# Performance work log

Hardware: AMD Instinct MI355X
Metric: run time of the kernel (lower is better)

Reference implementation:

```python
import jax, jax.numpy as jnp
import numpy as np

N_USER = 200000
N_TITEM = 200000  # sized >= N_USER because original code indexes ti_emb with user ids (faithful to source bug)
D = 256           # embed_dim
H = 128           # hidden = embed_dim // 2
N_HID = 2         # config.layers - 1 extra hidden blocks
B = 65536


def setup_inputs() -> dict:
    key = jax.random.key(0)
    ks = jax.random.split(key, 10)
    sc_d = 1.0 / np.sqrt(D)
    sc_h = 1.0 / np.sqrt(H)
    return {
        "user": jax.random.randint(ks[0], (B,), 0, N_USER),
        "item": jax.random.randint(ks[1], (B,), 0, 100000),
        "su_table": jax.random.normal(ks[2], (N_USER, D), jnp.float32) * 0.1,
        "ti_table": jax.random.normal(ks[3], (N_TITEM, D), jnp.float32) * 0.1,
        # 3 parallel MLP towers, stacked on leading axis t=3
        "Win": jax.random.normal(ks[4], (3, D, H), jnp.float32) * sc_d,
        "bin_": jnp.zeros((3, H), jnp.float32),
        "Wh": jax.random.normal(ks[5], (3, N_HID, H, H), jnp.float32) * sc_h,
        "bh": jnp.zeros((3, N_HID, H), jnp.float32),
        "Wout": jax.random.normal(ks[6], (3, H, D), jnp.float32) * sc_h,
        "bout": jnp.zeros((3, D), jnp.float32),
    }


def _towers(u, Win, bin_, Wh, bh, Wout, bout):
    # u: [B, D] -> x: [3, B, D] (three structurally identical MLP towers, batched)
    h = jax.nn.relu(jnp.einsum("bd,tdh->tbh", u, Win) + bin_[:, None, :])
    for i in range(N_HID):  # fixed small layer count
        h = jax.nn.relu(jnp.einsum("tbh,thk->tbk", h, Wh[:, i]) + bh[:, i][:, None, :])
    return jnp.einsum("tbh,thd->tbd", h, Wout) + bout[:, None, :]


def reference(user, item, su_table, ti_table, Win, bin_, Wh, bh, Wout, bout):
    u_embed = su_table[user]            # [B, D]
    i_key = ti_table[user]              # [B, D]  (faithful: original indexes ti_emb with `user`)
    x = _towers(u_embed, Win, bin_, Wh, bh, Wout, bout)   # [3, B, D]
    logits = jnp.einsum("tbd,bd->bt", x, i_key)           # [B, 3]
    attn = jax.nn.softmax(logits, axis=1)                 # [B, 3]
    fu = jnp.einsum("bt,tbd->bd", attn, x)                # [B, D]
    i_embed = ti_table[item]                              # [B, D]
    score = jnp.sum(fu * i_embed, axis=1)                 # [B]
    return score
```

## Files before the change

kernel.cpp:

```cpp
#include <hip/hip_runtime.h>
#include <hip/hip_bf16.h>
#include <stdint.h>

typedef __attribute__((ext_vector_type(8))) short short8;
typedef __attribute__((ext_vector_type(4))) float f32x4;

__device__ __forceinline__ short f2bf(float f) {
  union { float f; unsigned u; } x; x.f = f;
  unsigned r = (x.u + 0x7FFFu + ((x.u >> 16) & 1u)) >> 16;
  return (short)r;
}

__device__ __forceinline__ short8 cvt8(const float* p) {
  const float4 f0 = *(const float4*)p;
  const float4 f1 = *(const float4*)(p + 4);
  short8 r;
  r[0] = f2bf(f0.x); r[1] = f2bf(f0.y); r[2] = f2bf(f0.z); r[3] = f2bf(f0.w);
  r[4] = f2bf(f1.x); r[5] = f2bf(f1.y); r[6] = f2bf(f1.z); r[7] = f2bf(f1.w);
  return r;
}

__global__ __launch_bounds__(256) void pack_weights(
    const float* __restrict__ Win, const float* __restrict__ Wh,
    const float* __restrict__ Wout, short* __restrict__ o) {
  int gid = blockIdx.x * 256 + threadIdx.x;
  if (gid < 12288) {
    int t = gid / 4096, r = gid % 4096;
    int ks = r / 512, r2 = r % 512, nf = r2 / 64, l = r2 % 64;
    int n = nf * 16 + (l & 15);
    int kb = ks * 32 + (l >> 4) * 8;
#pragma unroll
    for (int i = 0; i < 8; ++i)
      o[gid * 8 + i] = f2bf(Win[(t * 256 + kb + i) * 128 + n]);
  } else if (gid < 24576) {
    int h = gid - 12288;
    int tl = h / 2048, r = h % 2048;
    int ks = r / 512, nf = (r % 512) / 64, l = r % 64;
    int n = nf * 16 + (l & 15);
    int kb = ks * 32 + (l >> 4) * 8;
#pragma unroll
    for (int i = 0; i < 8; ++i)
      o[98304 + h * 8 + i] = f2bf(Wh[(tl * 128 + kb + i) * 128 + n]);
  } else {
    int oo = gid - 24576;
    int t = oo / 4096, r = oo % 4096;
    int ks = r / 1024, nf = (r % 1024) / 64, l = r % 64;
    int n = nf * 16 + (l & 15);
    int kb = ks * 32 + (l >> 4) * 8;
#pragma unroll
    for (int i = 0; i < 8; ++i)
      o[196608 + oo * 8 + i] = f2bf(Wout[(t * 128 + kb + i) * 256 + n]);
  }
}

__global__ __launch_bounds__(256, 2) void fused_towers(
    const int* __restrict__ user, const int* __restrict__ item,
    const float* __restrict__ su, const float* __restrict__ ti,
    const float* __restrict__ bin, const float* __restrict__ bh,
    const float* __restrict__ bout, const short* __restrict__ wp,
    float* __restrict__ out) {
  __shared__ __align__(16) short sW[16384];
  __shared__ __align__(16) short sAct[16384];
  __shared__ float sL[3][64];
  __shared__ float sS[3][64];
  __shared__ int sUid[64];
  __shared__ int sItm[64];

  const int tid = threadIdx.x;
  const int w = tid >> 6, lane = tid & 63;
  const int ar = lane & 15, g = lane >> 4;
  const f32x4 fz = {0.f, 0.f, 0.f, 0.f};

  if (tid < 64) {
    sUid[tid] = user[blockIdx.x * 64 + tid];
    sItm[tid] = item[blockIdx.x * 64 + tid];
  }
  if (tid < 192) { (&sL[0][0])[tid] = 0.f; (&sS[0][0])[tid] = 0.f; }
  __syncthreads();

  const float* uptr[4];
#pragma unroll
  for (int m = 0; m < 4; ++m) uptr[m] = su + (size_t)sUid[m * 16 + ar] * 256;

  char* const Ha = (char*)sAct;
  char* const Hb = (char*)sAct + 16384;

  for (int t = 0; t < 3; ++t) {
    f32x4 acc[4][4];
#pragma unroll
    for (int m = 0; m < 4; ++m) { acc[m][0] = fz; acc[m][1] = fz; }
    for (int half = 0; half < 2; ++half) {
      __syncthreads();
      {
        const uint4* src = (const uint4*)(wp + t * 32768 + half * 16384);
        uint4* dst = (uint4*)sW;
#pragma unroll
        for (int i = 0; i < 8; ++i) dst[tid + i * 256] = src[tid + i * 256];
      }
      __syncthreads();
#pragma unroll
      for (int ksl = 0; ksl < 4; ++ksl) {
        const int K0 = half * 4 + ksl;
        short8 a[4];
#pragma unroll
        for (int m = 0; m < 4; ++m) a[m] = cvt8(uptr[m] + K0 * 32 + g * 8);
#pragma unroll
        for (int nfl = 0; nfl < 2; ++nfl) {
          const short8 b = *(const short8*)((const char*)sW + (ksl * 8 + w * 2 + nfl) * 1024 + lane * 16);
#pragma unroll
          for (int m = 0; m < 4; ++m)
            acc[m][nfl] = __builtin_amdgcn_mfma_f32_16x16x32_bf16(a[m], b, acc[m][nfl], 0, 0, 0);
        }
      }
    }
#pragma unroll
    for (int m = 0; m < 4; ++m)
#pragma unroll
      for (int nfl = 0; nfl < 2; ++nfl) {
        const int col = w * 32 + nfl * 16 + ar;
        const float bv = bin[t * 128 + col];
#pragma unroll
        for (int q = 0; q < 4; ++q) {
          const int r = m * 16 + g * 4 + q;
          const float v = fmaxf(acc[m][nfl][q] + bv, 0.f);
          *(short*)(Ha + r * 256 + ((col * 2) ^ ((r & 7) << 4))) = f2bf(v);
        }
      }
#pragma unroll
    for (int L = 0; L < 2; ++L) {
      char* const hin = L ? Hb : Ha;
      char* const hout = L ? Ha : Hb;
#pragma unroll
      for (int m = 0; m < 4; ++m) { acc[m][0] = fz; acc[m][1] = fz; }
      __syncthreads();
      {
        const uint4* src = (const uint4*)(wp + 98304 + (t * 2 + L) * 16384);
        uint4* dst = (uint4*)sW;
#pragma unroll
        for (int i = 0; i < 8; ++i) dst[tid + i * 256] = src[tid + i * 256];
      }
      __syncthreads();
#pragma unroll
      for (int ks = 0; ks < 4; ++ks) {
        short8 a[4];
#pragma unroll
        for (int m = 0; m < 4; ++m) {
          const int r = m * 16 + ar;
          a[m] = *(const short8*)(hin + r * 256 + ((ks * 64 + g * 16) ^ ((r & 7) << 4)));
        }
#pragma unroll
        for (int nfl = 0; nfl < 2; ++nfl) {
          const short8 b = *(const short8*)((const char*)sW + (ks * 8 + w * 2 + nfl) * 1024 + lane * 16);
#pragma unroll
          for (int m = 0; m < 4; ++m)
            acc[m][nfl] = __builtin_amdgcn_mfma_f32_16x16x32_bf16(a[m], b, acc[m][nfl], 0, 0, 0);
        }
      }
#pragma unroll
      for (int m = 0; m < 4; ++m)
#pragma unroll
        for (int nfl = 0; nfl < 2; ++nfl) {
          const int col = w * 32 + nfl * 16 + ar;
          const float bv = bh[(t * 2 + L) * 128 + col];
#pragma unroll
          for (int q = 0; q < 4; ++q) {
            const int r = m * 16 + g * 4 + q;
            const float v = fmaxf(acc[m][nfl][q] + bv, 0.f);
            *(short*)(hout + r * 256 + ((col * 2) ^ ((r & 7) << 4))) = f2bf(v);
          }
        }
    }
#pragma unroll
    for (int m = 0; m < 4; ++m)
#pragma unroll
      for (int n = 0; n < 4; ++n) acc[m][n] = fz;
    for (int half = 0; half < 2; ++half) {
      __syncthreads();
      {
        const uint4* src = (const uint4*)(wp + 196608 + t * 32768 + half * 16384);
        uint4* dst = (uint4*)sW;
#pragma unroll
        for (int i = 0; i < 8; ++i) dst[tid + i * 256] = src[tid + i * 256];
      }
      __syncthreads();
#pragma unroll
      for (int ksl = 0; ksl < 2; ++ksl) {
        const int K0 = half * 2 + ksl;
        short8 a[4];
#pragma unroll
        for (int m = 0; m < 4; ++m) {
          const int r = m * 16 + ar;
          a[m] = *(const short8*)(Ha + r * 256 + ((K0 * 64 + g * 16) ^ ((r & 7) << 4)));
        }
#pragma unroll
        for (int nfl = 0; nfl < 4; ++nfl) {
          const short8 b = *(const short8*)((const char*)sW + (ksl * 16 + w * 4 + nfl) * 1024 + lane * 16);
#pragma unroll
          for (int m = 0; m < 4; ++m)
            acc[m][nfl] = __builtin_amdgcn_mfma_f32_16x16x32_bf16(a[m], b, acc[m][nfl], 0, 0, 0);
        }
      }
    }
    float pl[16], ps[16];
#pragma unroll
    for (int i = 0; i < 16; ++i) { pl[i] = 0.f; ps[i] = 0.f; }
#pragma unroll
    for (int m = 0; m < 4; ++m)
#pragma unroll
      for (int nfl = 0; nfl < 4; ++nfl) {
        const int col = w * 64 + nfl * 16 + ar;
        const float bo = bout[t * 256 + col];
#pragma unroll
        for (int q = 0; q < 4; ++q) {
          const int r = m * 16 + g * 4 + q;
          const float x = acc[m][nfl][q] + bo;
          const float kv = ti[(size_t)sUid[r] * 256 + col];
          const float ev = ti[(size_t)sItm[r] * 256 + col];
          pl[m * 4 + q] += x * kv;
          ps[m * 4 + q] += x * ev;
        }
      }
#pragma unroll
    for (int i = 0; i < 16; ++i) {
      float a0 = pl[i], b0 = ps[i];
#pragma unroll
      for (int off = 1; off < 16; off <<= 1) {
        a0 += __shfl_xor(a0, off);
        b0 += __shfl_xor(b0, off);
      }
      pl[i] = a0; ps[i] = b0;
    }
    if (ar == 0) {
#pragma unroll
      for (int m = 0; m < 4; ++m)
#pragma unroll
        for (int q = 0; q < 4; ++q) {
          const int r = m * 16 + g * 4 + q;
          atomicAdd(&sL[t][r], pl[m * 4 + q]);
          atomicAdd(&sS[t][r], ps[m * 4 + q]);
        }
    }
  }
  __syncthreads();
  if (tid < 64) {
    const float l0 = sL[0][tid], l1 = sL[1][tid], l2 = sL[2][tid];
    const float mx = fmaxf(l0, fmaxf(l1, l2));
    const float e0 = __expf(l0 - mx), e1 = __expf(l1 - mx), e2 = __expf(l2 - mx);
    out[blockIdx.x * 64 + tid] =
        (e0 * sS[0][tid] + e1 * sS[1][tid] + e2 * sS[2][tid]) / (e0 + e1 + e2);
  }
}

extern "C" void kernel_launch(void* const* d_in, const int* in_sizes, int n_in,
                              void* d_out, int out_size, void* d_ws, size_t ws_size,
                              hipStream_t stream) {
  const int* user = (const int*)d_in[0];
  const int* item = (const int*)d_in[1];
  const float* su = (const float*)d_in[2];
  const float* ti = (const float*)d_in[3];
  const float* Win = (const float*)d_in[4];
  const float* bin = (const float*)d_in[5];
  const float* Wh = (const float*)d_in[6];
  const float* bh = (const float*)d_in[7];
  const float* Wout = (const float*)d_in[8];
  const float* bout = (const float*)d_in[9];
  float* out = (float*)d_out;
  short* ws = (short*)d_ws;

  hipLaunchKernelGGL(pack_weights, dim3(144), dim3(256), 0, stream, Win, Wh, Wout, ws);
  hipLaunchKernelGGL(fused_towers, dim3(1024), dim3(256), 0, stream,
                     user, item, su, ti, bin, bh, bout, (const short*)ws, out);
}
```

Measured before the change: 195.4 us.

## Read weight fragments straight from global memory and vectorize the epilogue dot products

Drops the shared-memory staging of packed weights. Each wave now loads its MFMA B fragments directly from global (L2-resident) memory, which frees 32KB of LDS and lets the launch bound rise to 4 blocks per SM. The output-layer result is written to LDS as bf16, and the two dot products against ti rows are done with coalesced float4 loads and a short shuffle reduction, replacing the scattered scalar gathers and LDS atomics. The costs are extra bf16 rounding of the tower output before the attention dot products, and repeated global weight loads per block.

```diff
diff --git a/kernel.cpp b/kernel.cpp
--- a/kernel.cpp
+++ b/kernel.cpp
@@ -10,7 +10,10 @@
   unsigned r = (x.u + 0x7FFFu + ((x.u >> 16) & 1u)) >> 16;
   return (short)r;
 }
-
+__device__ __forceinline__ float bf2f(short s) {
+  union { unsigned u; float f; } x; x.u = ((unsigned)(unsigned short)s) << 16;
+  return x.f;
+}
 __device__ __forceinline__ short8 cvt8(const float* p) {
   const float4 f0 = *(const float4*)p;
   const float4 f1 = *(const float4*)(p + 4);
@@ -53,14 +56,13 @@
   }
 }
 
-__global__ __launch_bounds__(256, 2) void fused_towers(
+__global__ __launch_bounds__(256, 4) void fused_towers(
     const int* __restrict__ user, const int* __restrict__ item,
     const float* __restrict__ su, const float* __restrict__ ti,
     const float* __restrict__ bin, const float* __restrict__ bh,
     const float* __restrict__ bout, const short* __restrict__ wp,
     float* __restrict__ out) {
-  __shared__ __align__(16) short sW[16384];
-  __shared__ __align__(16) short sAct[16384];
+  __shared__ __align__(16) char Act[32768];
   __shared__ float sL[3][64];
   __shared__ float sS[3][64];
   __shared__ int sUid[64];
@@ -75,42 +77,29 @@
     sUid[tid] = user[blockIdx.x * 64 + tid];
     sItm[tid] = item[blockIdx.x * 64 + tid];
   }
-  if (tid < 192) { (&sL[0][0])[tid] = 0.f; (&sS[0][0])[tid] = 0.f; }
   __syncthreads();
 
-  const float* uptr[4];
-#pragma unroll
-  for (int m = 0; m < 4; ++m) uptr[m] = su + (size_t)sUid[m * 16 + ar] * 256;
-
-  char* const Ha = (char*)sAct;
-  char* const Hb = (char*)sAct + 16384;
+  char* const Ha = Act;
+  char* const Hb = Act + 16384;
 
   for (int t = 0; t < 3; ++t) {
-    f32x4 acc[4][4];
-#pragma unroll
-    for (int m = 0; m < 4; ++m) { acc[m][0] = fz; acc[m][1] = fz; }
-    for (int half = 0; half < 2; ++half) {
-      __syncthreads();
-      {
-        const uint4* src = (const uint4*)(wp + t * 32768 + half * 16384);
-        uint4* dst = (uint4*)sW;
-#pragma unroll
-        for (int i = 0; i < 8; ++i) dst[tid + i * 256] = src[tid + i * 256];
-      }
-      __syncthreads();
-#pragma unroll
-      for (int ksl = 0; ksl < 4; ++ksl) {
-        const int K0 = half * 4 + ksl;
-        short8 a[4];
-#pragma unroll
-        for (int m = 0; m < 4; ++m) a[m] = cvt8(uptr[m] + K0 * 32 + g * 8);
-#pragma unroll
-        for (int nfl = 0; nfl < 2; ++nfl) {
-          const short8 b = *(const short8*)((const char*)sW + (ksl * 8 + w * 2 + nfl) * 1024 + lane * 16);
-#pragma unroll
-          for (int m = 0; m < 4; ++m)
-            acc[m][nfl] = __builtin_amdgcn_mfma_f32_16x16x32_bf16(a[m], b, acc[m][nfl], 0, 0, 0);
-        }
+    f32x4 acc2[4][2];
+#pragma unroll
+    for (int m = 0; m < 4; ++m) { acc2[m][0] = fz; acc2[m][1] = fz; }
+    const float* up[4];
+#pragma unroll
+    for (int m = 0; m < 4; ++m) up[m] = su + (size_t)sUid[m * 16 + ar] * 256;
+#pragma unroll
+    for (int K0 = 0; K0 < 8; ++K0) {
+      short8 a[4];
+#pragma unroll
+      for (int m = 0; m < 4; ++m) a[m] = cvt8(up[m] + K0 * 32 + g * 8);
+#pragma unroll
+      for (int nfl = 0; nfl < 2; ++nfl) {
+        const short8 b = *(const short8*)(wp + (size_t)((t * 8 + K0) * 8 + w * 2 + nfl) * 512 + lane * 8);
+#pragma unroll
+        for (int m = 0; m < 4; ++m)
+          acc2[m][nfl] = __builtin_amdgcn_mfma_f32_16x16x32_bf16(a[m], b, acc2[m][nfl], 0, 0, 0);
       }
     }
 #pragma unroll
@@ -122,24 +111,18 @@
 #pragma unroll
         for (int q = 0; q < 4; ++q) {
           const int r = m * 16 + g * 4 + q;
-          const float v = fmaxf(acc[m][nfl][q] + bv, 0.f);
+          const float v = fmaxf(acc2[m][nfl][q] + bv, 0.f);
           *(short*)(Ha + r * 256 + ((col * 2) ^ ((r & 7) << 4))) = f2bf(v);
         }
       }
+    __syncthreads();
+
 #pragma unroll
     for (int L = 0; L < 2; ++L) {
       char* const hin = L ? Hb : Ha;
       char* const hout = L ? Ha : Hb;
 #pragma unroll
-      for (int m = 0; m < 4; ++m) { acc[m][0] = fz; acc[m][1] = fz; }
-      __syncthreads();
-      {
-        const uint4* src = (const uint4*)(wp + 98304 + (t * 2 + L) * 16384);
-        uint4* dst = (uint4*)sW;
-#pragma unroll
-        for (int i = 0; i < 8; ++i) dst[tid + i * 256] = src[tid + i * 256];
-      }
-      __syncthreads();
+      for (int m = 0; m < 4; ++m) { acc2[m][0] = fz; acc2[m][1] = fz; }
 #pragma unroll
       for (int ks = 0; ks < 4; ++ks) {
         short8 a[4];
@@ -150,10 +133,10 @@
         }
 #pragma unroll
         for (int nfl = 0; nfl < 2; ++nfl) {
-          const short8 b = *(const short8*)((const char*)sW + (ks * 8 + w * 2 + nfl) * 1024 + lane * 16);
+          const short8 b = *(const short8*)(wp + 98304 + (size_t)(((t * 2 + L) * 4 + ks) * 8 + w * 2 + nfl) * 512 + lane * 8);
 #pragma unroll
           for (int m = 0; m < 4; ++m)
-            acc[m][nfl] = __builtin_amdgcn_mfma_f32_16x16x32_bf16(a[m], b, acc[m][nfl], 0, 0, 0);
+            acc2[m][nfl] = __builtin_amdgcn_mfma_f32_16x16x32_bf16(a[m], b, acc2[m][nfl], 0, 0, 0);
         }
       }
 #pragma unroll
@@ -165,45 +148,36 @@
 #pragma unroll
           for (int q = 0; q < 4; ++q) {
             const int r = m * 16 + g * 4 + q;
-            const float v = fmaxf(acc[m][nfl][q] + bv, 0.f);
+            const float v = fmaxf(acc2[m][nfl][q] + bv, 0.f);
             *(short*)(hout + r * 256 + ((col * 2) ^ ((r & 7) << 4))) = f2bf(v);
           }
         }
-    }
+      __syncthreads();
+    }
+
+    f32x4 acc4[4][4];
 #pragma unroll
     for (int m = 0; m < 4; ++m)
 #pragma unroll
-      for (int n = 0; n < 4; ++n) acc[m][n] = fz;
-    for (int half = 0; half < 2; ++half) {
-      __syncthreads();
-      {
-        const uint4* src = (const uint4*)(wp + 196608 + t * 32768 + half * 16384);
-        uint4* dst = (uint4*)sW;
-#pragma unroll
-        for (int i = 0; i < 8; ++i) dst[tid + i * 256] = src[tid + i * 256];
-      }
-      __syncthreads();
-#pragma unroll
-      for (int ksl = 0; ksl < 2; ++ksl) {
-        const int K0 = half * 2 + ksl;
-        short8 a[4];
-#pragma unroll
-        for (int m = 0; m < 4; ++m) {
-          const int r = m * 16 + ar;
-          a[m] = *(const short8*)(Ha + r * 256 + ((K0 * 64 + g * 16) ^ ((r & 7) << 4)));
-        }
-#pragma unroll
-        for (int nfl = 0; nfl < 4; ++nfl) {
-          const short8 b = *(const short8*)((const char*)sW + (ksl * 16 + w * 4 + nfl) * 1024 + lane * 16);
-#pragma unroll
-          for (int m = 0; m < 4; ++m)
-            acc[m][nfl] = __builtin_amdgcn_mfma_f32_16x16x32_bf16(a[m], b, acc[m][nfl], 0, 0, 0);
-        }
-      }
-    }
-    float pl[16], ps[16];
-#pragma unroll
-    for (int i = 0; i < 16; ++i) { pl[i] = 0.f; ps[i] = 0.f; }
+      for (int n = 0; n < 4; ++n) acc4[m][n] = fz;
+#pragma unroll
+    for (int K0 = 0; K0 < 4; ++K0) {
+      short8 a[4];
+#pragma unroll
+      for (int m = 0; m < 4; ++m) {
+        const int r = m * 16 + ar;
+        a[m] = *(const short8*)(Ha + r * 256 + ((K0 * 64 + g * 16) ^ ((r & 7) << 4)));
+      }
+#pragma unroll
+      for (int nfl = 0; nfl < 4; ++nfl) {
+        const short8 b = *(const short8*)(wp + 196608 + (size_t)((t * 4 + K0) * 16 + w * 4 + nfl) * 512 + lane * 8);
+#pragma unroll
+        for (int m = 0; m < 4; ++m)
+          acc4[m][nfl] = __builtin_amdgcn_mfma_f32_16x16x32_bf16(a[m], b, acc4[m][nfl], 0, 0, 0);
+      }
+    }
+    __syncthreads();
+
 #pragma unroll
     for (int m = 0; m < 4; ++m)
 #pragma unroll
@@ -213,35 +187,37 @@
 #pragma unroll
         for (int q = 0; q < 4; ++q) {
           const int r = m * 16 + g * 4 + q;
-          const float x = acc[m][nfl][q] + bo;
-          const float kv = ti[(size_t)sUid[r] * 256 + col];
-          const float ev = ti[(size_t)sItm[r] * 256 + col];
-          pl[m * 4 + q] += x * kv;
-          ps[m * 4 + q] += x * ev;
-        }
-      }
-#pragma unroll
-    for (int i = 0; i < 16; ++i) {
-      float a0 = pl[i], b0 = ps[i];
-#pragma unroll
-      for (int off = 1; off < 16; off <<= 1) {
-        a0 += __shfl_xor(a0, off);
-        b0 += __shfl_xor(b0, off);
-      }
-      pl[i] = a0; ps[i] = b0;
-    }
-    if (ar == 0) {
-#pragma unroll
-      for (int m = 0; m < 4; ++m)
-#pragma unroll
-        for (int q = 0; q < 4; ++q) {
-          const int r = m * 16 + g * 4 + q;
-          atomicAdd(&sL[t][r], pl[m * 4 + q]);
-          atomicAdd(&sS[t][r], ps[m * 4 + q]);
-        }
-    }
-  }
-  __syncthreads();
+          *(short*)(Act + r * 512 + ((col * 2) ^ ((r & 7) << 4))) = f2bf(acc4[m][nfl][q] + bo);
+        }
+      }
+    __syncthreads();
+
+    {
+      const int rr = tid >> 2, qq = tid & 3;
+      const float* kv = ti + (size_t)sUid[rr] * 256 + qq * 64;
+      const float* ev = ti + (size_t)sItm[rr] * 256 + qq * 64;
+      float l = 0.f, s = 0.f;
+#pragma unroll
+      for (int i = 0; i < 8; ++i) {
+        const short8 xv = *(const short8*)(Act + rr * 512 + ((qq * 128 + i * 16) ^ ((rr & 7) << 4)));
+        const float4 ka = *(const float4*)(kv + i * 8);
+        const float4 kb = *(const float4*)(kv + i * 8 + 4);
+        const float4 ea = *(const float4*)(ev + i * 8);
+        const float4 eb = *(const float4*)(ev + i * 8 + 4);
+        const float x0 = bf2f(xv[0]), x1 = bf2f(xv[1]), x2 = bf2f(xv[2]), x3 = bf2f(xv[3]);
+        const float x4 = bf2f(xv[4]), x5 = bf2f(xv[5]), x6 = bf2f(xv[6]), x7 = bf2f(xv[7]);
+        l += x0 * ka.x + x1 * ka.y + x2 * ka.z + x3 * ka.w
+           + x4 * kb.x + x5 * kb.y + x6 * kb.z + x7 * kb.w;
+        s += x0 * ea.x + x1 * ea.y + x2 * ea.z + x3 * ea.w
+           + x4 * eb.x + x5 * eb.y + x6 * eb.z + x7 * eb.w;
+      }
+      l += __shfl_xor(l, 1); l += __shfl_xor(l, 2);
+      s += __shfl_xor(s, 1); s += __shfl_xor(s, 2);
+      if (qq == 0) { sL[t][rr] = l; sS[t][rr] = s; }
+    }
+    __syncthreads();
+  }
+
   if (tid < 64) {
     const float l0 = sL[0][tid], l1 = sL[1][tid], l2 = sL[2][tid];
     const float mx = fmaxf(l0, fmaxf(l1, l2));
```

Result: slower. 341.2 us (+74.6%).

## Double-buffer weight staging with async global-to-LDS loads across all tower layers

Applied to the files above, without the earlier changes.

Replaces the synchronous copy of weights through registers into shared memory with `global_load_lds` direct-to-LDS loads. It stages 16KB weight pages into a two-slot buffer, prefetching the next page, including the next layer's or next tower's, while MFMAs run on the current one. The two ping-pong activation buffers are merged into one in-place buffer, which frees LDS, and the per-layer barriers are restructured around the prefetch. The bf16 conversion now uses the library intrinsic. The aim is to hide weight-load latency and cut barrier stalls. In exchange the kernel relies on barrier wait semantics for async LDS writes and adds more, smaller sync points.

```diff
diff --git a/kernel.cpp b/kernel.cpp
--- a/kernel.cpp
+++ b/kernel.cpp
@@ -6,11 +6,11 @@
 typedef __attribute__((ext_vector_type(4))) float f32x4;
 
 __device__ __forceinline__ short f2bf(float f) {
-  union { float f; unsigned u; } x; x.f = f;
-  unsigned r = (x.u + 0x7FFFu + ((x.u >> 16) & 1u)) >> 16;
-  return (short)r;
-}
-
+  __hip_bfloat16 h = __float2bfloat16(f);
+  union { __hip_bfloat16 h; unsigned short u; } c;
+  c.h = h;
+  return (short)c.u;
+}
 __device__ __forceinline__ short8 cvt8(const float* p) {
   const float4 f0 = *(const float4*)p;
   const float4 f1 = *(const float4*)(p + 4);
@@ -53,14 +53,26 @@
   }
 }
 
+__device__ __forceinline__ void stage16k(const short* __restrict__ wp,
+                                         char* lbuf, int pageBase, int tid) {
+  const char* g = (const char*)wp + (size_t)pageBase * 1024 + (size_t)tid * 16;
+  char* l = lbuf + (tid >> 6) * 1024;
+#pragma unroll
+  for (int r = 0; r < 4; ++r) {
+    __builtin_amdgcn_global_load_lds(
+        (const __attribute__((address_space(1))) void*)(g + r * 4096),
+        (__attribute__((address_space(3))) void*)(l + r * 4096), 16, 0, 0);
+  }
+}
+
 __global__ __launch_bounds__(256, 2) void fused_towers(
     const int* __restrict__ user, const int* __restrict__ item,
     const float* __restrict__ su, const float* __restrict__ ti,
     const float* __restrict__ bin, const float* __restrict__ bh,
     const float* __restrict__ bout, const short* __restrict__ wp,
     float* __restrict__ out) {
-  __shared__ __align__(16) short sW[16384];
-  __shared__ __align__(16) short sAct[16384];
+  __shared__ __align__(16) char WB[2][16384];
+  __shared__ __align__(16) char Act[16384];
   __shared__ float sL[3][64];
   __shared__ float sS[3][64];
   __shared__ int sUid[64];
@@ -69,6 +81,7 @@
   const int tid = threadIdx.x;
   const int w = tid >> 6, lane = tid & 63;
   const int ar = lane & 15, g = lane >> 4;
+  const int swzA = (ar & 7) << 4;
   const f32x4 fz = {0.f, 0.f, 0.f, 0.f};
 
   if (tid < 64) {
@@ -76,42 +89,41 @@
     sItm[tid] = item[blockIdx.x * 64 + tid];
   }
   if (tid < 192) { (&sL[0][0])[tid] = 0.f; (&sS[0][0])[tid] = 0.f; }
+  stage16k(wp, WB[0], 0, tid);
   __syncthreads();
-
-  const float* uptr[4];
-#pragma unroll
-  for (int m = 0; m < 4; ++m) uptr[m] = su + (size_t)sUid[m * 16 + ar] * 256;
-
-  char* const Ha = (char*)sAct;
-  char* const Hb = (char*)sAct + 16384;
+  int cur = 0;
 
   for (int t = 0; t < 3; ++t) {
-    f32x4 acc[4][4];
+    const int b1 = t * 64;
+    const int b2 = 192 + (t * 2) * 32;
+    const int b3 = 192 + (t * 2 + 1) * 32;
+    const int b4 = 384 + t * 64;
+    const float* up[4];
+#pragma unroll
+    for (int m = 0; m < 4; ++m) up[m] = su + (size_t)sUid[m * 16 + ar] * 256;
+
+    f32x4 acc[4][2];
 #pragma unroll
     for (int m = 0; m < 4; ++m) { acc[m][0] = fz; acc[m][1] = fz; }
-    for (int half = 0; half < 2; ++half) {
-      __syncthreads();
-      {
-        const uint4* src = (const uint4*)(wp + t * 32768 + half * 16384);
-        uint4* dst = (uint4*)sW;
-#pragma unroll
-        for (int i = 0; i < 8; ++i) dst[tid + i * 256] = src[tid + i * 256];
-      }
-      __syncthreads();
-#pragma unroll
-      for (int ksl = 0; ksl < 4; ++ksl) {
-        const int K0 = half * 4 + ksl;
+    for (int c = 0; c < 4; ++c) {
+      stage16k(wp, WB[cur ^ 1], (c < 3) ? (b1 + (c + 1) * 16) : b2, tid);
+      const char* wb = WB[cur];
+#pragma unroll
+      for (int ksl = 0; ksl < 2; ++ksl) {
+        const int K0 = c * 2 + ksl;
         short8 a[4];
 #pragma unroll
-        for (int m = 0; m < 4; ++m) a[m] = cvt8(uptr[m] + K0 * 32 + g * 8);
+        for (int m = 0; m < 4; ++m) a[m] = cvt8(up[m] + K0 * 32 + g * 8);
 #pragma unroll
         for (int nfl = 0; nfl < 2; ++nfl) {
-          const short8 b = *(const short8*)((const char*)sW + (ksl * 8 + w * 2 + nfl) * 1024 + lane * 16);
+          const short8 b = *(const short8*)(wb + (ksl * 8 + w * 2 + nfl) * 1024 + lane * 16);
 #pragma unroll
           for (int m = 0; m < 4; ++m)
             acc[m][nfl] = __builtin_amdgcn_mfma_f32_16x16x32_bf16(a[m], b, acc[m][nfl], 0, 0, 0);
         }
       }
+      __syncthreads();
+      cur ^= 1;
     }
 #pragma unroll
     for (int m = 0; m < 4; ++m)
@@ -123,38 +135,39 @@
         for (int q = 0; q < 4; ++q) {
           const int r = m * 16 + g * 4 + q;
           const float v = fmaxf(acc[m][nfl][q] + bv, 0.f);
-          *(short*)(Ha + r * 256 + ((col * 2) ^ ((r & 7) << 4))) = f2bf(v);
-        }
-      }
+          *(short*)(Act + r * 256 + ((col * 2) ^ ((r & 7) << 4))) = f2bf(v);
+        }
+      }
+    __syncthreads();
+
 #pragma unroll
     for (int L = 0; L < 2; ++L) {
-      char* const hin = L ? Hb : Ha;
-      char* const hout = L ? Ha : Hb;
+      const int bb = L ? b3 : b2;
+      const int nx0 = L ? b4 : b3;
 #pragma unroll
       for (int m = 0; m < 4; ++m) { acc[m][0] = fz; acc[m][1] = fz; }
-      __syncthreads();
-      {
-        const uint4* src = (const uint4*)(wp + 98304 + (t * 2 + L) * 16384);
-        uint4* dst = (uint4*)sW;
-#pragma unroll
-        for (int i = 0; i < 8; ++i) dst[tid + i * 256] = src[tid + i * 256];
-      }
-      __syncthreads();
-#pragma unroll
-      for (int ks = 0; ks < 4; ++ks) {
-        short8 a[4];
-#pragma unroll
-        for (int m = 0; m < 4; ++m) {
-          const int r = m * 16 + ar;
-          a[m] = *(const short8*)(hin + r * 256 + ((ks * 64 + g * 16) ^ ((r & 7) << 4)));
-        }
-#pragma unroll
-        for (int nfl = 0; nfl < 2; ++nfl) {
-          const short8 b = *(const short8*)((const char*)sW + (ks * 8 + w * 2 + nfl) * 1024 + lane * 16);
-#pragma unroll
-          for (int m = 0; m < 4; ++m)
-            acc[m][nfl] = __builtin_amdgcn_mfma_f32_16x16x32_bf16(a[m], b, acc[m][nfl], 0, 0, 0);
-        }
+      for (int c = 0; c < 2; ++c) {
+        stage16k(wp, WB[cur ^ 1], (c < 1) ? (bb + 16) : nx0, tid);
+        const char* wb = WB[cur];
+#pragma unroll
+        for (int csl = 0; csl < 2; ++csl) {
+          const int ks = c * 2 + csl;
+          short8 a[4];
+#pragma unroll
+          for (int m = 0; m < 4; ++m) {
+            const int r = m * 16 + ar;
+            a[m] = *(const short8*)(Act + r * 256 + ((ks * 64 + g * 16) ^ swzA));
+          }
+#pragma unroll
+          for (int nfl = 0; nfl < 2; ++nfl) {
+            const short8 b = *(const short8*)(wb + (csl * 8 + w * 2 + nfl) * 1024 + lane * 16);
+#pragma unroll
+            for (int m = 0; m < 4; ++m)
+              acc[m][nfl] = __builtin_amdgcn_mfma_f32_16x16x32_bf16(a[m], b, acc[m][nfl], 0, 0, 0);
+          }
+        }
+        __syncthreads();
+        cur ^= 1;
       }
 #pragma unroll
       for (int m = 0; m < 4; ++m)
@@ -166,41 +179,39 @@
           for (int q = 0; q < 4; ++q) {
             const int r = m * 16 + g * 4 + q;
             const float v = fmaxf(acc[m][nfl][q] + bv, 0.f);
-            *(short*)(hout + r * 256 + ((col * 2) ^ ((r & 7) << 4))) = f2bf(v);
+            *(short*)(Act + r * 256 + ((col * 2) ^ ((r & 7) << 4))) = f2bf(v);
           }
         }
-    }
+      __syncthreads();
+    }
+
+    f32x4 acc4[4][4];
 #pragma unroll
     for (int m = 0; m < 4; ++m)
 #pragma unroll
-      for (int n = 0; n < 4; ++n) acc[m][n] = fz;
-    for (int half = 0; half < 2; ++half) {
+      for (int n = 0; n < 4; ++n) acc4[m][n] = fz;
+    for (int c = 0; c < 4; ++c) {
+      const bool last = (t == 2) && (c == 3);
+      if (!last)
+        stage16k(wp, WB[cur ^ 1], (c < 3) ? (b4 + (c + 1) * 16) : ((t + 1) * 64), tid);
+      const char* wb = WB[cur];
+      short8 a4[4];
+#pragma unroll
+      for (int m = 0; m < 4; ++m) {
+        const int r = m * 16 + ar;
+        a4[m] = *(const short8*)(Act + r * 256 + ((c * 64 + g * 16) ^ swzA));
+      }
+#pragma unroll
+      for (int nfl = 0; nfl < 4; ++nfl) {
+        const short8 b = *(const short8*)(wb + (w * 4 + nfl) * 1024 + lane * 16);
+#pragma unroll
+        for (int m = 0; m < 4; ++m)
+          acc4[m][nfl] = __builtin_amdgcn_mfma_f32_16x16x32_bf16(a4[m], b, acc4[m][nfl], 0, 0, 0);
+      }
       __syncthreads();
-      {
-        const uint4* src = (const uint4*)(wp + 196608 + t * 32768 + half * 16384);
-        uint4* dst = (uint4*)sW;
-#pragma unroll
-        for (int i = 0; i < 8; ++i) dst[tid + i * 256] = src[tid + i * 256];
-      }
-      __syncthreads();
-#pragma unroll
-      for (int ksl = 0; ksl < 2; ++ksl) {
-        const int K0 = half * 2 + ksl;
-        short8 a[4];
-#pragma unroll
-        for (int m = 0; m < 4; ++m) {
-          const int r = m * 16 + ar;
-          a[m] = *(const short8*)(Ha + r * 256 + ((K0 * 64 + g * 16) ^ ((r & 7) << 4)));
-        }
-#pragma unroll
-        for (int nfl = 0; nfl < 4; ++nfl) {
-          const short8 b = *(const short8*)((const char*)sW + (ksl * 16 + w * 4 + nfl) * 1024 + lane * 16);
-#pragma unroll
-          for (int m = 0; m < 4; ++m)
-            acc[m][nfl] = __builtin_amdgcn_mfma_f32_16x16x32_bf16(a[m], b, acc[m][nfl], 0, 0, 0);
-        }
-      }
-    }
+      cur ^= 1;
+    }
+
     float pl[16], ps[16];
 #pragma unroll
     for (int i = 0; i < 16; ++i) { pl[i] = 0.f; ps[i] = 0.f; }
@@ -213,7 +224,7 @@
 #pragma unroll
         for (int q = 0; q < 4; ++q) {
           const int r = m * 16 + g * 4 + q;
-          const float x = acc[m][nfl][q] + bo;
+          const float x = acc4[m][nfl][q] + bo;
           const float kv = ti[(size_t)sUid[r] * 256 + col];
           const float ev = ti[(size_t)sItm[r] * 256 + col];
           pl[m * 4 + q] += x * kv;
@@ -242,6 +253,7 @@
     }
   }
   __syncthreads();
+
   if (tid < 64) {
     const float l0 = sL[0][tid], l1 = sL[1][tid], l2 = sL[2][tid];
     const float mx = fmaxf(l0, fmaxf(l1, l2));
```

Result: slower. 246.6 us (+26.2%).
